# Kernel optimization log

Hardware: AMD Instinct MI355X
Metric: run time of the kernel (lower is better)

The kernel has to match this reference:

```python
import jax, jax.numpy as jnp
import numpy as np

NODE_N = 23
SEQ_LEN = 35
N_HEADS = 3
BN_EPS = 1e-5


def _normalize_digraph(A):
    # column-normalize: A @ diag(1/deg) (st-gcn tools.normalize_digraph)
    Dl = A.sum(0)
    inv = np.where(Dl > 0, 1.0 / np.where(Dl > 0, Dl, 1.0), 0.0)
    return A * inv[None, :]


def _build_A_ske():
    n = NODE_N
    bone = [[0, 2], [1, 2], [0, 3], [3, 6], [6, 9], [1, 4], [4, 7], [7, 10],
            [2, 5], [5, 8], [8, 12], [12, 15], [15, 17], [17, 19], [19, 21],
            [8, 13], [13, 16], [16, 18], [18, 20], [20, 22], [8, 11], [11, 14]]
    A_in = np.zeros((n, n), np.float64)
    A_out = np.zeros((n, n), np.float64)
    for i, j in bone:
        A_in[i, j] = 1.0
        A_out[j, i] = 1.0
    A_self = np.eye(n, dtype=np.float64)
    return np.stack([_normalize_digraph(A_in), _normalize_digraph(A_out), A_self]).astype(np.float32)


def setup_inputs() -> dict:
    key = jax.random.key(0)
    ks = jax.random.split(key, 12)
    b, c, o, n, l = 256, 64, 64, NODE_N, SEQ_LEN
    stdv = 1.0 / np.sqrt(n)           # reset_parameters: 1/sqrt(att.size(2)) = 1/sqrt(n)
    cbound = 1.0 / np.sqrt(c)         # conv2d 1x1 default init bound (fan_in = in_c)
    u = lambda k, shape, bnd: jax.random.uniform(k, shape, jnp.float32, -bnd, bnd)
    return {
        "x": jax.random.normal(ks[0], (b, c, n, l), jnp.float32),
        "cw1": u(ks[1], (N_HEADS, o, c), cbound),
        "cb1": u(ks[2], (N_HEADS, o), cbound),
        "cw2": u(ks[3], (N_HEADS, o, c), cbound),
        "cb2": u(ks[4], (N_HEADS, o), cbound),
        "bn_gamma": jnp.ones((N_HEADS, n * n), jnp.float32),
        "bn_beta": jnp.zeros((N_HEADS, n * n), jnp.float32),
        "mw": u(ks[5], (N_HEADS, o, c), cbound),
        "mb": u(ks[6], (N_HEADS, o), cbound),
        "att": jnp.full((N_HEADS, n, n), 1e-6, jnp.float32),
        "A_ske": jnp.asarray(_build_A_ske()),
        "weight_seq": u(ks[7], (l, l), stdv),
        "bias": u(ks[8], (l,), stdv),
    }


def reference(x, cw1, cb1, cw2, cb2, bn_gamma, bn_beta, mw, mb, att, A_ske, weight_seq, bias):
    b, c, n, l = x.shape
    o = cw1.shape[1]
    xp = jnp.transpose(x, (0, 1, 3, 2))                      # [b,c,l,n]

    # --- A_adp heads (vectorized across 3 heads) ---
    o1 = jnp.einsum('hoc,bcln->bholn', cw1, xp) + cb1[None, :, :, None, None]
    o2 = jnp.einsum('hoc,bcln->bholn', cw2, xp) + cb2[None, :, :, None, None]
    o1 = o1.reshape(b, N_HEADS, o * l, n)
    o2 = o2.reshape(b, N_HEADS, o * l, n)
    att_m = jnp.einsum('bhkm,bhkn->bhmn', o2, o1) / (o * l)  # [b,3,n,n]

    # BatchNorm1d over flattened n*n features, batch statistics (training mode)
    flat = att_m.reshape(b, N_HEADS, n * n)
    mean = flat.mean(axis=0)                                  # [3,n*n]
    var = flat.var(axis=0)                                    # biased, as torch BN
    flat = (flat - mean) / jnp.sqrt(var + BN_EPS) * bn_gamma + bn_beta
    A_adp = jax.nn.softmax(flat.reshape(b, N_HEADS, n, n), axis=-2)
    # dropout is identity in eval mode

    # --- graph convolution per head ---
    A = A_ske[None] + att[None] + A_adp                       # [b,3,n,n]
    support = jnp.einsum('bcln,bhnm->bhclm', xp, A)           # [b,3,c,l,n]
    head = jnp.einsum('hoc,bhclm->bholm', mw, support) + mb[None, :, :, None, None]
    gcn = jnp.transpose(head.sum(axis=1), (0, 1, 3, 2))       # [b,o,n,l]

    out = jnp.einsum('bonl,lm->bonm', gcn, weight_seq) + bias
    return out
```

## Files before the change

### kernel.cpp

```cpp
#include <hip/hip_runtime.h>
#include <hip/hip_bf16.h>

typedef __hip_bfloat16 bf16;
typedef __attribute__((ext_vector_type(8))) short bf16x8;
typedef __attribute__((ext_vector_type(4))) float f32x4;
typedef __attribute__((ext_vector_type(4))) unsigned short us4;
typedef __attribute__((ext_vector_type(8))) unsigned short us8;

#define NB   256
#define NN   23
#define NL   35
#define NNL  805
#define CNL  51520
#define NSQ  529
#define HF   1587
#define NCN  1472

#define OFF_W     0
#define OFF_U1    12288
#define OFF_U2    12480
#define OFF_S     12672
#define OFF_ATTM  12800
#define OFF_MEAN  419072
#define OFF_RSTD  420672
#define OFF_A     422272
#define OFF_MWH   828544
#define OFF_MWL   834688
#define OFF_MBS   840832
#define OFF_XTB   840960

__device__ inline unsigned short bfh(float x) {
    unsigned u = __float_as_uint(x);
    return (unsigned short)((u + 0x7FFFu + ((u >> 16) & 1u)) >> 16);
}
__device__ inline float bfh2f(unsigned short h) {
    return __uint_as_float(((unsigned)h) << 16);
}

__global__ __launch_bounds__(1024) void k_xt(const float* __restrict__ x,
                                             float* __restrict__ ws) {
    int b = blockIdx.x, t = threadIdx.x;
    __shared__ float sx[64 * 23 * 18];
    const float* xb = x + b * CNL;
    unsigned short* xo = (unsigned short*)(ws + OFF_XTB) + (size_t)b * NL * 2944;
    for (int lh = 0; lh < 2; lh++) {
        int l0 = lh * 18, Lc = lh ? 17 : 18;
        if (lh) __syncthreads();
        for (int i = t; i < 1472 * Lc; i += 1024) {
            int cn = i / Lc, li = i - cn * Lc;
            sx[cn * 18 + li] = xb[cn * 35 + l0 + li];
        }
        __syncthreads();
        for (int item = t; item < 184 * Lc; item += 1024) {
            int li = item / 184, rem = item - li * 184;
            int n = rem >> 3, k = rem & 7;
            us8 hi, lo;
            #pragma unroll
            for (int e = 0; e < 8; e++) {
                float v = sx[((8 * k + e) * 23 + n) * 18 + li];
                unsigned short hb = bfh(v);
                hi[e] = hb;
                lo[e] = bfh(v - bfh2f(hb));
            }
            unsigned short* dst = xo + (size_t)(l0 + li) * 2944 + n * 64 + 8 * k;
            *(us8*)(dst) = hi;
            *(us8*)(dst + 1472) = lo;
        }
    }
}

__global__ __launch_bounds__(256) void k_prep(const float* __restrict__ cw1,
                                              const float* __restrict__ cb1,
                                              const float* __restrict__ cw2,
                                              const float* __restrict__ cb2,
                                              const float* __restrict__ mw,
                                              const float* __restrict__ mb,
                                              float* __restrict__ ws) {
    int h = blockIdx.x, t = threadIdx.x;
    __shared__ float s1[4096], s2[4096];
    if (h < 3) {
        for (int i = t; i < 4096; i += 256) {
            s1[i] = cw1[h * 4096 + i];
            s2[i] = cw2[h * 4096 + i];
        }
        __syncthreads();
        for (int i = t; i < 4096; i += 256) {
            int c2 = i >> 6, c1 = i & 63;
            float acc = 0.f;
            for (int o = 0; o < 64; o++) acc += s2[o * 64 + c2] * s1[o * 64 + c1];
            ws[OFF_W + h * 4096 + i] = acc;
        }
        if (t < 64) {
            float a = 0.f, b2 = 0.f;
            for (int o = 0; o < 64; o++) {
                a  += cb2[h * 64 + o] * s1[o * 64 + t];
                b2 += cb1[h * 64 + o] * s2[o * 64 + t];
            }
            ws[OFF_U1 + h * 64 + t] = a;
            ws[OFF_U2 + h * 64 + t] = b2;
        }
        if (t == 0) {
            float a = 0.f;
            for (int o = 0; o < 64; o++) a += cb1[h * 64 + o] * cb2[h * 64 + o];
            ws[OFF_S + h] = a;
        }
    } else {
        unsigned short* mh = (unsigned short*)(ws + OFF_MWH);
        unsigned short* ml = (unsigned short*)(ws + OFF_MWL);
        for (int i = t; i < 12288; i += 256) {
            float v = mw[i];
            unsigned short hb = bfh(v);
            mh[i] = hb;
            ml[i] = bfh(v - bfh2f(hb));
        }
        if (t < 64) ws[OFF_MBS + t] = mb[t] + mb[64 + t] + mb[128 + t];
    }
}

__global__ __launch_bounds__(256) void k_attm(float* __restrict__ ws) {
    const int b = blockIdx.x, h = blockIdx.y, t = threadIdx.x;
    const int lane = t & 63;
    const int w = __builtin_amdgcn_readfirstlane(t >> 6);
    const int lg = lane >> 4;
    const int lr = lane & 15;

    __shared__ unsigned short sXh[2][32 * 72];
    __shared__ unsigned short sXl[2][32 * 72];
    __shared__ unsigned short sPh[32 * 72];
    __shared__ unsigned short sPl[32 * 72];
    __shared__ float sxs[64 * 25];
    __shared__ float sA1[23], sA2[23];

    const unsigned short* xthl = (const unsigned short*)(ws + OFF_XTB);

    bf16x8 wh[2], wl[2];
    {
        const float* Wg = ws + OFF_W + h * 4096 + (16 * w + lr) * 64;
        #pragma unroll
        for (int s = 0; s < 2; s++) {
            const float* p = Wg + 32 * s + 8 * lg;
            float4 v0 = *(const float4*)(p);
            float4 v1 = *(const float4*)(p + 4);
            float vv[8] = {v0.x, v0.y, v0.z, v0.w, v1.x, v1.y, v1.z, v1.w};
            #pragma unroll
            for (int e = 0; e < 8; e++) {
                unsigned short hb = bfh(vv[e]);
                wh[s][e] = (short)hb;
                wl[s][e] = (short)bfh(vv[e] - bfh2f(hb));
            }
        }
    }

    const int j1 = t;
    const int p1 = j1 / 184, r1 = j1 - p1 * 184;
    const int n1 = r1 >> 3, k1 = r1 & 7;
    unsigned short* d1 = (p1 ? sXl[0] : sXh[0]) + n1 * 72 + 8 * k1;
    const int j2 = 256 + t;
    const int r2 = j2 - 184;
    const int n2 = r2 >> 3, k2 = r2 & 7;
    unsigned short* d2 = sXl[0] + n2 * 72 + 8 * k2;

    const int mt = w >> 1, nt = w & 1;
    f32x4 attC = {0.f, 0.f, 0.f, 0.f};
    float xa1[8] = {0, 0, 0, 0, 0, 0, 0, 0};
    float xa2[8] = {0, 0, 0, 0, 0, 0, 0, 0};

    #pragma unroll 1
    for (int l = 0; l < NL; l++) {
        const int cur = l & 1;
        {
            const us8* g = (const us8*)(xthl + (size_t)(b * NL + l) * 2944);
            us8 v1 = g[j1];
            *(us8*)(d1 + cur * 2304) = v1;
            #pragma unroll
            for (int e = 0; e < 8; e++) xa1[e] += bfh2f(v1[e]);
            if (t < 112) {
                us8 v2 = g[j2];
                *(us8*)(d2 + cur * 2304) = v2;
                #pragma unroll
                for (int e = 0; e < 8; e++) xa2[e] += bfh2f(v2[e]);
            }
        }
        __syncthreads();

        const unsigned short* xh = sXh[cur];
        const unsigned short* xl = sXl[cur];

        f32x4 pc[2];
        #pragma unroll
        for (int ntt = 0; ntt < 2; ntt++) {
            f32x4 c = {0.f, 0.f, 0.f, 0.f};
            #pragma unroll
            for (int s = 0; s < 2; s++) {
                int off = (ntt * 16 + lr) * 72 + 32 * s + 8 * lg;
                bf16x8 bh = *(const bf16x8*)(xh + off);
                bf16x8 bl = *(const bf16x8*)(xl + off);
                c = __builtin_amdgcn_mfma_f32_16x16x32_bf16(wh[s], bh, c, 0, 0, 0);
                c = __builtin_amdgcn_mfma_f32_16x16x32_bf16(wh[s], bl, c, 0, 0, 0);
                c = __builtin_amdgcn_mfma_f32_16x16x32_bf16(wl[s], bh, c, 0, 0, 0);
            }
            pc[ntt] = c;
        }
        #pragma unroll
        for (int ntt = 0; ntt < 2; ntt++) {
            int n = ntt * 16 + lr;
            int c2 = 16 * w + 4 * lg;
            us4 ph4, pl4;
            #pragma unroll
            for (int r = 0; r < 4; r++) {
                float v = pc[ntt][r];
                unsigned short hb = bfh(v);
                ph4[r] = hb;
                pl4[r] = bfh(v - bfh2f(hb));
            }
            *(us4*)(sPh + n * 72 + c2) = ph4;
            *(us4*)(sPl + n * 72 + c2) = pl4;
        }
        __syncthreads();

        #pragma unroll
        for (int s = 0; s < 2; s++) {
            int aoff = (mt * 16 + lr) * 72 + 32 * s + 8 * lg;
            int boff = (nt * 16 + lr) * 72 + 32 * s + 8 * lg;
            bf16x8 ah = *(const bf16x8*)(xh + aoff);
            bf16x8 al = *(const bf16x8*)(xl + aoff);
            bf16x8 bh = *(const bf16x8*)(sPh + boff);
            bf16x8 bl = *(const bf16x8*)(sPl + boff);
            attC = __builtin_amdgcn_mfma_f32_16x16x32_bf16(ah, bh, attC, 0, 0, 0);
            attC = __builtin_amdgcn_mfma_f32_16x16x32_bf16(ah, bl, attC, 0, 0, 0);
            attC = __builtin_amdgcn_mfma_f32_16x16x32_bf16(al, bh, attC, 0, 0, 0);
        }
    }

    if (t < 184) {
        #pragma unroll
        for (int e = 0; e < 8; e++) sxs[(8 * k1 + e) * 25 + n1] = xa1[e];
    }
    __syncthreads();
    if (t >= 184) {
        #pragma unroll
        for (int e = 0; e < 8; e++) sxs[(8 * k1 + e) * 25 + n1] += xa1[e];
    }
    if (t < 112) {
        #pragma unroll
        for (int e = 0; e < 8; e++) sxs[(8 * k2 + e) * 25 + n2] += xa2[e];
    }
    __syncthreads();
    if (t < 23) {
        float a = 0.f;
        const float* u = ws + OFF_U1 + h * 64;
        for (int c = 0; c < 64; c++) a += u[c] * sxs[c * 25 + t];
        sA1[t] = a;
    } else if (t >= 32 && t < 55) {
        int n = t - 32;
        float a = 0.f;
        const float* u = ws + OFF_U2 + h * 64;
        for (int c = 0; c < 64; c++) a += u[c] * sxs[c * 25 + n];
        sA2[n] = a;
    }
    __syncthreads();

    float sh = ws[OFF_S + h];
    float* o = ws + OFF_ATTM + (size_t)b * HF + h * NSQ;
    int n = nt * 16 + lr;
    if (n < 23) {
        #pragma unroll
        for (int r = 0; r < 4; r++) {
            int m = mt * 16 + 4 * lg + r;
            if (m < 23)
                o[m * 23 + n] = (attC[r] + sA1[n] + sA2[m] + 35.f * sh) * (1.f / 2240.f);
        }
    }
}

__global__ __launch_bounds__(256) void k_bn(float* __restrict__ ws) {
    int f = blockIdx.x * 256 + threadIdx.x;
    if (f >= HF) return;
    const float* p = ws + OFF_ATTM + f;
    float s = 0.f, s2 = 0.f;
    for (int b = 0; b < NB; b++) {
        float v = p[b * HF];
        s += v; s2 += v * v;
    }
    float mean = s * (1.f / 256.f);
    float var  = s2 * (1.f / 256.f) - mean * mean;
    ws[OFF_MEAN + f] = mean;
    ws[OFF_RSTD + f] = rsqrtf(var + 1e-5f);
}

__global__ __launch_bounds__(256) void k_adp(const float* __restrict__ gamma,
                                             const float* __restrict__ beta,
                                             const float* __restrict__ att,
                                             const float* __restrict__ aske,
                                             float* __restrict__ ws) {
    int b = blockIdx.x, h = blockIdx.y, t = threadIdx.x;
    __shared__ float sv[529];
    const float* am   = ws + OFF_ATTM + b * HF + h * NSQ;
    const float* mean = ws + OFF_MEAN + h * NSQ;
    const float* rstd = ws + OFF_RSTD + h * NSQ;
    for (int i = t; i < 529; i += 256) {
        sv[i] = (am[i] - mean[i]) * rstd[i] * gamma[h * NSQ + i] + beta[h * NSQ + i];
    }
    __syncthreads();
    if (t < 23) {
        float mx = -1e30f;
        #pragma unroll
        for (int m = 0; m < 23; m++) mx = fmaxf(mx, sv[m * 23 + t]);
        float e[23];
        float sum = 0.f;
        #pragma unroll
        for (int m = 0; m < 23; m++) {
            float v = __expf(sv[m * 23 + t] - mx);
            e[m] = v; sum += v;
        }
        float inv = 1.f / sum;
        #pragma unroll
        for (int m = 0; m < 23; m++) sv[m * 23 + t] = e[m] * inv;
    }
    __syncthreads();
    float* o = ws + OFF_A + b * HF + h * NSQ;
    for (int i = t; i < 529; i += 256) {
        o[i] = sv[i] + aske[h * NSQ + i] + att[h * NSQ + i];
    }
}

__global__ __launch_bounds__(512, 2) void k_fused(float* __restrict__ ws,
                                                  const float* __restrict__ wseq,
                                                  const float* __restrict__ biasp,
                                                  float* __restrict__ out) {
    const int b = blockIdx.x, t = threadIdx.x;
    const int lane = t & 63;
    const int w = __builtin_amdgcn_readfirstlane(t >> 6);
    const int lg = lane >> 4, lr = lane & 15;
    const int nt = w >> 2, ot = w & 3;
    const int ot2 = w >> 1, mt = w & 1;

    __shared__ __align__(16) unsigned short sXh[32 * 72], sXl[32 * 72];
    __shared__ __align__(16) unsigned short sAT[3][2][32 * 40];
    __shared__ __align__(16) unsigned short sT[3][64 * 40];
    __shared__ __align__(16) unsigned short sY[1472 * 36];
    __shared__ __align__(16) unsigned short sWTh[48 * 40], sWTl[48 * 40];
    __shared__ float sWt[3 * 35];
    __shared__ float sBias[35];

    const unsigned short* xthl = (const unsigned short*)(ws + OFF_XTB);
    const float* Ab  = ws + OFF_A + (size_t)b * HF;

    for (int i = t; i < 9 * 72; i += 512) {
        sXh[23 * 72 + i] = 0;
        sXl[23 * 72 + i] = 0;
    }
    for (int i = t; i < 3 * 1280; i += 512) {
        int h = i / 1280, r2 = i - h * 1280, m = r2 / 40, n = r2 - m * 40;
        float v = (n < 23 && m < 23) ? Ab[h * 529 + n * 23 + m] : 0.f;
        unsigned short hb = bfh(v);
        sAT[h][0][m * 40 + n] = hb;
        sAT[h][1][m * 40 + n] = bfh(v - bfh2f(hb));
    }
    for (int i = t; i < 48 * 40; i += 512) {
        int lp = i / 40, l = i - lp * 40;
        float v = (lp < 35 && l < 32) ? wseq[l * 35 + lp] : 0.f;
        unsigned short hb = bfh(v);
        sWTh[i] = hb;
        sWTl[i] = bfh(v - bfh2f(hb));
    }
    if (t < 105) sWt[t] = wseq[(32 + t / 35) * 35 + (t % 35)];
    if (t >= 128 && t < 163) sBias[t - 128] = biasp[t - 128];

    const unsigned short* mwh = (const unsigned short*)(ws + OFF_MWH);
    const unsigned short* mwl = (const unsigned short*)(ws + OFF_MWL);
    bf16x8 fwh[3][2], fwl[3][2];
    #pragma unroll
    for (int h = 0; h < 3; h++)
        #pragma unroll
        for (int s = 0; s < 2; s++) {
            int off = h * 4096 + (16 * ot + lr) * 64 + 32 * s + 8 * lg;
            fwh[h][s] = *(const bf16x8*)(mwh + off);
            fwl[h][s] = *(const bf16x8*)(mwl + off);
        }
    float4 mbsv = *(const float4*)(ws + OFF_MBS + 16 * ot2 + 4 * lg);
    float mb4[4] = {mbsv.x, mbsv.y, mbsv.z, mbsv.w};

    const int p1 = t / 184, r1 = t - p1 * 184;
    const int n1 = r1 >> 3, k1 = r1 & 7;
    unsigned short* d1 = (p1 ? sXl : sXh) + n1 * 72 + 8 * k1;

    const f32x4 zf = {0.f, 0.f, 0.f, 0.f};

    #pragma unroll 1
    for (int l = 0; l < NL; l++) {
        if (t < 368) {
            const us8* g = (const us8*)(xthl + (size_t)(b * NL + l) * 2944);
            *(us8*)d1 = g[t];
        }
        __syncthreads();

        bf16x8 xh0 = *(const bf16x8*)(sXh + (16 * nt + lr) * 72 + 8 * lg);
        bf16x8 xh1 = *(const bf16x8*)(sXh + (16 * nt + lr) * 72 + 32 + 8 * lg);
        bf16x8 xl0 = *(const bf16x8*)(sXl + (16 * nt + lr) * 72 + 8 * lg);
        bf16x8 xl1 = *(const bf16x8*)(sXl + (16 * nt + lr) * 72 + 32 + 8 * lg);
        #pragma unroll
        for (int h = 0; h < 3; h++) {
            f32x4 cH = __builtin_amdgcn_mfma_f32_16x16x32_bf16(xh0, fwh[h][0], zf, 0, 0, 0);
            cH = __builtin_amdgcn_mfma_f32_16x16x32_bf16(xh1, fwh[h][1], cH, 0, 0, 0);
            f32x4 cC = __builtin_amdgcn_mfma_f32_16x16x32_bf16(xh0, fwl[h][0], zf, 0, 0, 0);
            cC = __builtin_amdgcn_mfma_f32_16x16x32_bf16(xh1, fwl[h][1], cC, 0, 0, 0);
            cC = __builtin_amdgcn_mfma_f32_16x16x32_bf16(xl0, fwh[h][0], cC, 0, 0, 0);
            cC = __builtin_amdgcn_mfma_f32_16x16x32_bf16(xl1, fwh[h][1], cC, 0, 0, 0);
            us4 t4;
            #pragma unroll
            for (int r = 0; r < 4; r++) t4[r] = bfh(cH[r] + cC[r]);
            *(us4*)(&sT[h][(16 * ot + lr) * 40 + 16 * nt + 4 * lg]) = t4;
        }
        __syncthreads();

        f32x4 Yh = zf, Yc = zf;
        #pragma unroll
        for (int h = 0; h < 3; h++) {
            bf16x8 ta = *(const bf16x8*)(&sT[h][(16 * ot2 + lr) * 40 + 8 * lg]);
            bf16x8 ah = *(const bf16x8*)(&sAT[h][0][(16 * mt + lr) * 40 + 8 * lg]);
            bf16x8 al = *(const bf16x8*)(&sAT[h][1][(16 * mt + lr) * 40 + 8 * lg]);
            Yh = __builtin_amdgcn_mfma_f32_16x16x32_bf16(ta, ah, Yh, 0, 0, 0);
            Yc = __builtin_amdgcn_mfma_f32_16x16x32_bf16(ta, al, Yc, 0, 0, 0);
        }
        int m = 16 * mt + lr;
        if (m < 23) {
            #pragma unroll
            for (int r = 0; r < 4; r++) {
                int o = 16 * ot2 + 4 * lg + r;
                float yv = Yh[r] + Yc[r] + mb4[r];
                sY[(o * 23 + m) * 36 + l] = bfh(yv);
            }
        }
    }
    __syncthreads();

    #pragma unroll 1
    for (int tt = w; tt < 276; tt += 8) {
        int pt = tt / 3, lt = tt - pt * 3;
        int pA = 16 * pt + lr;
        us4 a0 = *(const us4*)(sY + pA * 36 + 8 * lg);
        us4 a1 = *(const us4*)(sY + pA * 36 + 8 * lg + 4);
        union { bf16x8 v; us4 h2[2]; } au;
        au.h2[0] = a0; au.h2[1] = a1;
        bf16x8 wbh = *(const bf16x8*)(sWTh + (16 * lt + lr) * 40 + 8 * lg);
        bf16x8 wbl = *(const bf16x8*)(sWTl + (16 * lt + lr) * 40 + 8 * lg);
        f32x4 c0 = __builtin_amdgcn_mfma_f32_16x16x32_bf16(au.v, wbh, zf, 0, 0, 0);
        f32x4 c1 = __builtin_amdgcn_mfma_f32_16x16x32_bf16(au.v, wbl, zf, 0, 0, 0);
        int lpc = 16 * lt + lr;
        if (lpc < 35) {
            float wt0 = sWt[lpc], wt1 = sWt[35 + lpc], wt2 = sWt[70 + lpc];
            float bv = sBias[lpc];
            #pragma unroll
            for (int r = 0; r < 4; r++) {
                int pr = 16 * pt + 4 * lg + r;
                us4 yt = *(const us4*)(sY + pr * 36 + 32);
                float v = c0[r] + c1[r] + bv
                        + bfh2f(yt[0]) * wt0 + bfh2f(yt[1]) * wt1 + bfh2f(yt[2]) * wt2;
                out[((size_t)b * 1472 + pr) * 35 + lpc] = v;
            }
        }
    }
}

extern "C" void kernel_launch(void* const* d_in, const int* in_sizes, int n_in,
                              void* d_out, int out_size, void* d_ws, size_t ws_size,
                              hipStream_t stream) {
    const float* x    = (const float*)d_in[0];
    const float* cw1  = (const float*)d_in[1];
    const float* cb1  = (const float*)d_in[2];
    const float* cw2  = (const float*)d_in[3];
    const float* cb2  = (const float*)d_in[4];
    const float* gam  = (const float*)d_in[5];
    const float* bet  = (const float*)d_in[6];
    const float* mw   = (const float*)d_in[7];
    const float* mb   = (const float*)d_in[8];
    const float* att  = (const float*)d_in[9];
    const float* aske = (const float*)d_in[10];
    const float* wsq  = (const float*)d_in[11];
    const float* bias = (const float*)d_in[12];
    float* ws = (float*)d_ws;
    float* out = (float*)d_out;

    hipLaunchKernelGGL(k_prep, dim3(4),       dim3(256),  0, stream, cw1, cb1, cw2, cb2, mw, mb, ws);
    hipLaunchKernelGGL(k_xt,   dim3(256),     dim3(1024), 0, stream, x, ws);
    hipLaunchKernelGGL(k_attm, dim3(256, 3),  dim3(256),  0, stream, ws);
    hipLaunchKernelGGL(k_bn,   dim3(7),       dim3(256),  0, stream, ws);
    hipLaunchKernelGGL(k_adp,  dim3(256, 3),  dim3(256),  0, stream, gam, bet, att, aske, ws);
    hipLaunchKernelGGL(k_fused, dim3(256),    dim3(512),  0, stream, ws, wsq, bias, out);
}
```

Before: 275.0 us.

## Prefetch next time step in attm/fused loops, parallelize BN reduction, pad LDS strides

```diff
diff --git a/kernel.cpp b/kernel.cpp
--- a/kernel.cpp
+++ b/kernel.cpp
@@ -35,6 +35,10 @@
 }
 __device__ inline float bfh2f(unsigned short h) {
     return __uint_as_float(((unsigned)h) << 16);
+}
+__device__ inline unsigned short bf16rn(float x) {
+    __hip_bfloat16 h = __float2bfloat16(x);
+    return __builtin_bit_cast(unsigned short, h);
 }
 
 __global__ __launch_bounds__(1024) void k_xt(const float* __restrict__ x,
@@ -165,23 +169,31 @@
     float xa1[8] = {0, 0, 0, 0, 0, 0, 0, 0};
     float xa2[8] = {0, 0, 0, 0, 0, 0, 0, 0};
 
+    {
+        const us8* g = (const us8*)(xthl + (size_t)(b * NL) * 2944);
+        us8 v1 = g[j1];
+        *(us8*)(d1) = v1;
+        #pragma unroll
+        for (int e = 0; e < 8; e++) xa1[e] += bfh2f(v1[e]);
+        if (t < 112) {
+            us8 v2 = g[j2];
+            *(us8*)(d2) = v2;
+            #pragma unroll
+            for (int e = 0; e < 8; e++) xa2[e] += bfh2f(v2[e]);
+        }
+    }
+
     #pragma unroll 1
     for (int l = 0; l < NL; l++) {
         const int cur = l & 1;
-        {
-            const us8* g = (const us8*)(xthl + (size_t)(b * NL + l) * 2944);
-            us8 v1 = g[j1];
-            *(us8*)(d1 + cur * 2304) = v1;
-            #pragma unroll
-            for (int e = 0; e < 8; e++) xa1[e] += bfh2f(v1[e]);
-            if (t < 112) {
-                us8 v2 = g[j2];
-                *(us8*)(d2 + cur * 2304) = v2;
-                #pragma unroll
-                for (int e = 0; e < 8; e++) xa2[e] += bfh2f(v2[e]);
-            }
-        }
         __syncthreads();
+
+        us8 vn1, vn2;
+        if (l < NL - 1) {
+            const us8* g = (const us8*)(xthl + (size_t)(b * NL + l + 1) * 2944);
+            vn1 = g[j1];
+            if (t < 112) vn2 = g[j2];
+        }
 
         const unsigned short* xh = sXh[cur];
         const unsigned short* xl = sXl[cur];
@@ -209,12 +221,23 @@
             #pragma unroll
             for (int r = 0; r < 4; r++) {
                 float v = pc[ntt][r];
-                unsigned short hb = bfh(v);
+                unsigned short hb = bf16rn(v);
                 ph4[r] = hb;
-                pl4[r] = bfh(v - bfh2f(hb));
+                pl4[r] = bf16rn(v - bfh2f(hb));
             }
             *(us4*)(sPh + n * 72 + c2) = ph4;
             *(us4*)(sPl + n * 72 + c2) = pl4;
+        }
+
+        if (l < NL - 1) {
+            *(us8*)(d1 + (cur ^ 1) * 2304) = vn1;
+            #pragma unroll
+            for (int e = 0; e < 8; e++) xa1[e] += bfh2f(vn1[e]);
+            if (t < 112) {
+                *(us8*)(d2 + (cur ^ 1) * 2304) = vn2;
+                #pragma unroll
+                for (int e = 0; e < 8; e++) xa2[e] += bfh2f(vn2[e]);
+            }
         }
         __syncthreads();
 
@@ -273,19 +296,30 @@
     }
 }
 
-__global__ __launch_bounds__(256) void k_bn(float* __restrict__ ws) {
-    int f = blockIdx.x * 256 + threadIdx.x;
-    if (f >= HF) return;
-    const float* p = ws + OFF_ATTM + f;
+__global__ __launch_bounds__(512) void k_bn(float* __restrict__ ws) {
+    int t = threadIdx.x;
+    int fi = t & 63, bg = t >> 6;
+    int f = blockIdx.x * 64 + fi;
+    __shared__ float rs[8][64], rs2[8][64];
     float s = 0.f, s2 = 0.f;
-    for (int b = 0; b < NB; b++) {
-        float v = p[b * HF];
-        s += v; s2 += v * v;
-    }
-    float mean = s * (1.f / 256.f);
-    float var  = s2 * (1.f / 256.f) - mean * mean;
-    ws[OFF_MEAN + f] = mean;
-    ws[OFF_RSTD + f] = rsqrtf(var + 1e-5f);
+    if (f < HF) {
+        const float* p = ws + OFF_ATTM + f + (size_t)bg * 32 * HF;
+        for (int b = 0; b < 32; b++) {
+            float v = p[b * HF];
+            s += v; s2 += v * v;
+        }
+    }
+    rs[bg][fi] = s; rs2[bg][fi] = s2;
+    __syncthreads();
+    if (bg == 0 && f < HF) {
+        float ts = 0.f, ts2 = 0.f;
+        #pragma unroll
+        for (int g = 0; g < 8; g++) { ts += rs[g][fi]; ts2 += rs2[g][fi]; }
+        float mean = ts * (1.f / 256.f);
+        float var  = ts2 * (1.f / 256.f) - mean * mean;
+        ws[OFF_MEAN + f] = mean;
+        ws[OFF_RSTD + f] = rsqrtf(var + 1e-5f);
+    }
 }
 
 __global__ __launch_bounds__(256) void k_adp(const float* __restrict__ gamma,
@@ -324,6 +358,8 @@
     }
 }
 
+#define SYS 38
+#define STS 44
 __global__ __launch_bounds__(512, 2) void k_fused(float* __restrict__ ws,
                                                   const float* __restrict__ wseq,
                                                   const float* __restrict__ biasp,
@@ -337,8 +373,8 @@
 
     __shared__ __align__(16) unsigned short sXh[32 * 72], sXl[32 * 72];
     __shared__ __align__(16) unsigned short sAT[3][2][32 * 40];
-    __shared__ __align__(16) unsigned short sT[3][64 * 40];
-    __shared__ __align__(16) unsigned short sY[1472 * 36];
+    __shared__ __align__(16) unsigned short sT[3][64 * STS];
+    __shared__ __align__(16) unsigned short sY[1472 * SYS];
     __shared__ __align__(16) unsigned short sWTh[48 * 40], sWTl[48 * 40];
     __shared__ float sWt[3 * 35];
     __shared__ float sBias[35];
@@ -387,13 +423,20 @@
 
     const f32x4 zf = {0.f, 0.f, 0.f, 0.f};
 
+    if (t < 368) {
+        const us8* g = (const us8*)(xthl + (size_t)(b * NL) * 2944);
+        *(us8*)d1 = g[t];
+    }
+
     #pragma unroll 1
     for (int l = 0; l < NL; l++) {
-        if (t < 368) {
-            const us8* g = (const us8*)(xthl + (size_t)(b * NL + l) * 2944);
-            *(us8*)d1 = g[t];
-        }
         __syncthreads();
+
+        us8 vn;
+        if (l < NL - 1 && t < 368) {
+            const us8* g = (const us8*)(xthl + (size_t)(b * NL + l + 1) * 2944);
+            vn = g[t];
+        }
 
         bf16x8 xh0 = *(const bf16x8*)(sXh + (16 * nt + lr) * 72 + 8 * lg);
         bf16x8 xh1 = *(const bf16x8*)(sXh + (16 * nt + lr) * 72 + 32 + 8 * lg);
@@ -409,19 +452,21 @@
             cC = __builtin_amdgcn_mfma_f32_16x16x32_bf16(xl1, fwh[h][1], cC, 0, 0, 0);
             us4 t4;
             #pragma unroll
-            for (int r = 0; r < 4; r++) t4[r] = bfh(cH[r] + cC[r]);
-            *(us4*)(&sT[h][(16 * ot + lr) * 40 + 16 * nt + 4 * lg]) = t4;
+            for (int r = 0; r < 4; r++) t4[r] = bf16rn(cH[r] + cC[r]);
+            *(us4*)(&sT[h][(16 * ot + lr) * STS + 16 * nt + 4 * lg]) = t4;
         }
         __syncthreads();
 
         f32x4 Yh = zf, Yc = zf;
         #pragma unroll
         for (int h = 0; h < 3; h++) {
-            bf16x8 ta = *(const bf16x8*)(&sT[h][(16 * ot2 + lr) * 40 + 8 * lg]);
+            union { bf16x8 v; us4 q[2]; } tu;
+            tu.q[0] = *(const us4*)(&sT[h][(16 * ot2 + lr) * STS + 8 * lg]);
+            tu.q[1] = *(const us4*)(&sT[h][(16 * ot2 + lr) * STS + 8 * lg + 4]);
             bf16x8 ah = *(const bf16x8*)(&sAT[h][0][(16 * mt + lr) * 40 + 8 * lg]);
             bf16x8 al = *(const bf16x8*)(&sAT[h][1][(16 * mt + lr) * 40 + 8 * lg]);
-            Yh = __builtin_amdgcn_mfma_f32_16x16x32_bf16(ta, ah, Yh, 0, 0, 0);
-            Yc = __builtin_amdgcn_mfma_f32_16x16x32_bf16(ta, al, Yc, 0, 0, 0);
+            Yh = __builtin_amdgcn_mfma_f32_16x16x32_bf16(tu.v, ah, Yh, 0, 0, 0);
+            Yc = __builtin_amdgcn_mfma_f32_16x16x32_bf16(tu.v, al, Yc, 0, 0, 0);
         }
         int m = 16 * mt + lr;
         if (m < 23) {
@@ -429,9 +474,11 @@
             for (int r = 0; r < 4; r++) {
                 int o = 16 * ot2 + 4 * lg + r;
                 float yv = Yh[r] + Yc[r] + mb4[r];
-                sY[(o * 23 + m) * 36 + l] = bfh(yv);
-            }
-        }
+                sY[(o * 23 + m) * SYS + l] = bf16rn(yv);
+            }
+        }
+
+        if (l < NL - 1 && t < 368) *(us8*)d1 = vn;
     }
     __syncthreads();
 
@@ -439,10 +486,12 @@
     for (int tt = w; tt < 276; tt += 8) {
         int pt = tt / 3, lt = tt - pt * 3;
         int pA = 16 * pt + lr;
-        us4 a0 = *(const us4*)(sY + pA * 36 + 8 * lg);
-        us4 a1 = *(const us4*)(sY + pA * 36 + 8 * lg + 4);
-        union { bf16x8 v; us4 h2[2]; } au;
-        au.h2[0] = a0; au.h2[1] = a1;
+        const unsigned short* yb = sY + pA * SYS + 8 * lg;
+        union { bf16x8 v; unsigned u[4]; } au;
+        au.u[0] = *(const unsigned*)(yb);
+        au.u[1] = *(const unsigned*)(yb + 2);
+        au.u[2] = *(const unsigned*)(yb + 4);
+        au.u[3] = *(const unsigned*)(yb + 6);
         bf16x8 wbh = *(const bf16x8*)(sWTh + (16 * lt + lr) * 40 + 8 * lg);
         bf16x8 wbl = *(const bf16x8*)(sWTl + (16 * lt + lr) * 40 + 8 * lg);
         f32x4 c0 = __builtin_amdgcn_mfma_f32_16x16x32_bf16(au.v, wbh, zf, 0, 0, 0);
@@ -454,9 +503,13 @@
             #pragma unroll
             for (int r = 0; r < 4; r++) {
                 int pr = 16 * pt + 4 * lg + r;
-                us4 yt = *(const us4*)(sY + pr * 36 + 32);
+                const unsigned short* yt = sY + pr * SYS + 32;
+                unsigned t0 = *(const unsigned*)(yt);
+                unsigned t1 = *(const unsigned*)(yt + 2);
                 float v = c0[r] + c1[r] + bv
-                        + bfh2f(yt[0]) * wt0 + bfh2f(yt[1]) * wt1 + bfh2f(yt[2]) * wt2;
+                        + bfh2f((unsigned short)(t0 & 0xffff)) * wt0
+                        + bfh2f((unsigned short)(t0 >> 16))    * wt1
+                        + bfh2f((unsigned short)(t1 & 0xffff)) * wt2;
                 out[((size_t)b * 1472 + pr) * 35 + lpc] = v;
             }
         }
@@ -485,7 +538,7 @@
     hipLaunchKernelGGL(k_prep, dim3(4),       dim3(256),  0, stream, cw1, cb1, cw2, cb2, mw, mb, ws);
     hipLaunchKernelGGL(k_xt,   dim3(256),     dim3(1024), 0, stream, x, ws);
     hipLaunchKernelGGL(k_attm, dim3(256, 3),  dim3(256),  0, stream, ws);
-    hipLaunchKernelGGL(k_bn,   dim3(7),       dim3(256),  0, stream, ws);
+    hipLaunchKernelGGL(k_bn,   dim3(25),      dim3(512),  0, stream, ws);
     hipLaunchKernelGGL(k_adp,  dim3(256, 3),  dim3(256),  0, stream, gam, bet, att, aske, ws);
     hipLaunchKernelGGL(k_fused, dim3(256),    dim3(512),  0, stream, ws, wsq, bias, out);
 }
```

After: 253.0 us. 1.09x faster.
